# Kernel tuning notes

Measured on AMD Instinct MI355X. Metric: run time of the kernel, lower is better.

Reference implementation:

```python
import jax, jax.numpy as jnp
import numpy as np

N = 512
NQ = 8
SIGMA = 1.0
NORM_FACTOR = 90.4756
NC = NORM_FACTOR / (2.0 * np.pi)  # norm_const = norm_factor / twopi


def make_kernels(r, sigma, nc):
    # Gaussian-screened Coulomb kernel g(r) = erf(a r)/r, a = 1/(sigma*sqrt(2)),
    # and its Cartesian tensor derivatives D1..D4 (D_n = (1/r d/dr)^n g).
    n = r.shape[0]
    d = r[None, :, :] - r[:, None, :]          # d[i,j] = r_j - r_i  [n,n,3]
    eye = jnp.eye(n, dtype=bool)
    r2 = jnp.sum(d * d, axis=-1)
    rr = jnp.sqrt(jnp.where(eye, 1.0, r2))     # safe diagonal
    a = 1.0 / (sigma * np.sqrt(2.0))
    a2 = a * a
    E = jax.scipy.special.erf(a * rr)
    G = (2.0 * a / np.sqrt(np.pi)) * jnp.exp(-a2 * rr * rr)
    ir = 1.0 / rr
    ir2 = ir * ir; ir3 = ir2 * ir; ir4 = ir2 * ir2; ir5 = ir4 * ir
    ir6 = ir4 * ir2; ir7 = ir6 * ir; ir8 = ir4 * ir4; ir9 = ir8 * ir
    off = jnp.where(eye, 0.0, 1.0).astype(r.dtype)  # remove self interaction
    g  = E * ir * off
    D1 = (G * ir2 - E * ir3) * off
    D2 = (3.0 * E * ir5 - 3.0 * G * ir4 - 2.0 * a2 * G * ir2) * off
    D3 = (-15.0 * E * ir7 + 15.0 * G * ir6 + 10.0 * a2 * G * ir4
          + 4.0 * a2 * a2 * G * ir2) * off
    D4 = (105.0 * E * ir9 - 105.0 * G * ir8 - 70.0 * a2 * G * ir6
          - 28.0 * a2 * a2 * G * ir4 - 8.0 * a2 * a2 * a2 * G * ir2) * off
    I3 = jnp.eye(3, dtype=r.dtype)
    f_qq = nc * g                                        # [n,n]
    f_qu = -nc * D1[..., None] * d                       # [n,n,3]
    dd = d[..., :, None] * d[..., None, :]               # [n,n,3,3]
    f_uu = nc * (D2[..., None, None] * dd + D1[..., None, None] * I3)
    ddd = dd[..., None] * d[..., None, None, :]          # [n,n,3,3,3]
    s3 = (jnp.einsum('ab,ijc->ijabc', I3, d)
          + jnp.einsum('ac,ijb->ijabc', I3, d)
          + jnp.einsum('bc,ija->ijabc', I3, d))
    f_Qu = nc * (D3[..., None, None, None] * ddd + D2[..., None, None, None] * s3)
    dddd = ddd[..., None] * d[:, :, None, None, None, :]  # [n,n,3,3,3,3]
    s6 = (jnp.einsum('ab,ijcd->ijabcd', I3, dd)
          + jnp.einsum('ac,ijbd->ijabcd', I3, dd)
          + jnp.einsum('ad,ijbc->ijabcd', I3, dd)
          + jnp.einsum('bc,ijad->ijabcd', I3, dd)
          + jnp.einsum('bd,ijac->ijabcd', I3, dd)
          + jnp.einsum('cd,ijab->ijabcd', I3, dd))
    iso = (jnp.einsum('ab,cd->abcd', I3, I3)
           + jnp.einsum('ac,bd->abcd', I3, I3)
           + jnp.einsum('ad,bc->abcd', I3, I3))
    f_QQ = nc * (D4[..., None, None, None, None] * dddd
                 + D3[..., None, None, None, None] * s6
                 + D2[..., None, None, None, None] * iso)
    return f_qq, f_qu, f_uu, f_Qu, f_QQ


def ewald_realspace(q, r, u, quad, kappa, alpha):
    f_qq, f_qu, f_uu, f_Qu, f_QQ = make_kernels(r, SIGMA, NC)
    # charge-charge
    e_phi = jnp.einsum('iq,ij->jq', q, f_qq)
    pot = 0.5 * jnp.einsum('iq,iq->q', e_phi, q)
    # charge-dipole
    e_phi_u = jnp.einsum('iqc,ijc->jq', u, f_qu)
    e_phi = e_phi + e_phi_u
    pot = pot + jnp.einsum('iq,iq->q', e_phi_u, q)
    # dipole-dipole
    E_u = jnp.einsum('ijcd,iqc->jqd', f_uu, u)
    pot = pot - 0.5 * jnp.einsum('iqc,iqc->q', u, E_u)
    # quadrupole terms
    e_phi_Q = 0.5 * jnp.einsum('iqab,ijab->jq', quad, f_uu)
    E_Q = -0.5 * jnp.einsum('iqab,ijabc->jqc', quad, f_Qu)
    e_phi = e_phi + e_phi_Q
    pot = pot + jnp.einsum('iq,iq->q', q, e_phi_Q)
    QQ = jnp.einsum('ijabcd,jqcd->iqab', f_QQ, quad)
    pot = pot + 0.125 * jnp.einsum('iqab,iqab->q', quad, QQ)
    pot = pot - jnp.einsum('iqc,iqc->q', u, E_Q)
    # induced charges (kappa)
    q_induced = -kappa * e_phi
    pot = pot + 0.5 * jnp.sum(e_phi * q_induced, axis=0)
    # field and induced dipoles (alpha, scalar polarizability)
    e_field = jnp.einsum('iq,ijc->jqc', q, f_qu) + E_u + E_Q
    u_induced = e_field * alpha[..., None]
    pot = pot - 0.5 * jnp.sum(e_field * u_induced, axis=(0, 2))
    return pot.sum().reshape(-1), q_induced, u_induced


def setup_inputs():
    key = jax.random.key(0)
    ks = jax.random.split(key, 6)
    r = jax.random.normal(ks[0], (N, 3), jnp.float32) * 5.0
    q = jax.random.normal(ks[1], (N, NQ), jnp.float32)
    u = jax.random.normal(ks[2], (N, NQ, 3), jnp.float32)
    quad = jax.random.normal(ks[3], (N, NQ, 3, 3), jnp.float32)
    kappa = jax.random.uniform(ks[4], (N, NQ), jnp.float32)
    alpha = jax.random.uniform(ks[5], (N, NQ), jnp.float32)
    cell = jnp.zeros((1, 3, 3), jnp.float32)   # det < 1e-6 -> realspace branch
    batch = jnp.zeros((N,), jnp.int32)         # single system
    return {'q': q, 'r': r, 'cell': cell, 'batch': batch, 'u': u,
            'quad': quad, 'kappa': kappa, 'alpha': alpha}


def reference(q, r, cell, batch, u, quad, kappa, alpha):
    # cell is zero (det < 1e-6) and batch is a single graph -> realspace path
    return ewald_realspace(q, r, u, quad, kappa, alpha)
```

## Files before the change

### kernel.cpp

```cpp
#include <hip/hip_runtime.h>
#include <math.h>

#define NA 512
#define NQC 8

#define NCf ((float)(90.4756 / 6.28318530717958647692))
#define A_ERF 0.70710678118654752f
#define G_COEF 0.79788456080286536f

typedef float v2f __attribute__((ext_vector_type(2)));

__global__ __launch_bounds__(512)
void main_kernel(const float* __restrict__ qarr,
                 const float* __restrict__ rarr,
                 const float* __restrict__ uarr,
                 const float* __restrict__ quadarr,
                 const float* __restrict__ kaparr,
                 const float* __restrict__ alparr,
                 float* __restrict__ out,
                 float* __restrict__ potpart) {
    const int j    = blockIdx.x;
    const int tid  = threadIdx.x;
    const int qch  = tid & 7;
    const int lane = tid & 63;
    const int wv   = tid >> 6;

    __shared__ float sCo[8][64][8];

    const float rjx = rarr[j*3+0], rjy = rarr[j*3+1], rjz = rarr[j*3+2];

    const int jq = j * NQC + qch;
    const float* Qj = quadarr + (size_t)jq * 9;
    const float jxx = Qj[0], jyy = Qj[4], jzz = Qj[8];
    const float jxy = 0.5f*(Qj[1]+Qj[3]);
    const float jxz = 0.5f*(Qj[2]+Qj[6]);
    const float jyz = 0.5f*(Qj[5]+Qj[7]);
    const float jtq = jxx + jyy + jzz;

    {
        const int myi = ((lane >> 3) << 6) + (wv << 3) + (lane & 7);
        const float mdx = rjx - rarr[myi*3+0];
        const float mdy = rjy - rarr[myi*3+1];
        const float mdz = rjz - rarr[myi*3+2];
        float r2 = mdx*mdx + mdy*mdy + mdz*mdz;
        const bool diag = (myi == j);
        if (diag) r2 = 1.0f;
        const float ir  = rsqrtf(r2);
        const float rr  = r2 * ir;
        const float x   = A_ERF * rr;
        const float E2  = __expf(-0.5f * r2);
        const float G   = G_COEF * E2;
        const float t   = __builtin_amdgcn_rcpf(fmaf(0.3275911f, x, 1.0f));
        const float pol = t*(0.254829592f + t*(-0.284496736f + t*(1.421413741f
                         + t*(-1.453152027f + t*1.061405429f))));
        const float E   = fmaf(-pol, E2, 1.0f);
        const float ir2 = ir * ir;
        const float ir4 = ir2 * ir2;
        const float g   = E * ir;
        const float GmG = G - g;
        const float nco = diag ? 0.0f : NCf;
        float4* slot = (float4*)&sCo[wv][lane][0];
        slot[0] = make_float4(nco * g,
                              nco * ir2 * GmG,
                              nco * ir2 * (-3.0f*ir2*GmG - G),
                              nco * ir2 * (15.0f*ir4*GmG + 5.0f*G*ir2 + G));
        slot[1] = make_float4(nco * ir2 * (-105.0f*ir4*ir2*GmG - 35.0f*G*ir4
                                           - 7.0f*G*ir2 - G),
                              mdx, mdy, mdz);
    }

    v2f e0 = 0.f, eph = 0.f;
    v2f Gx = 0.f, Gy = 0.f, Gz = 0.f;
    v2f Hx = 0.f, Hy = 0.f, Hz = 0.f;
    v2f pQQ = 0.f;

    #pragma unroll
    for (int k2 = 0; k2 < 4; ++k2) {
        const int iq0 = (2*k2) * 512 + tid;
        const int iq1 = iq0 + 512;
        const int p0  = ((2*k2) << 3) + (lane >> 3);
        const int p1  = p0 + 8;

        const float4 ca0 = *(const float4*)&sCo[wv][p0][0];
        const float4 cb0 = *(const float4*)&sCo[wv][p0][4];
        const float4 ca1 = *(const float4*)&sCo[wv][p1][0];
        const float4 cb1 = *(const float4*)&sCo[wv][p1][4];
        const v2f c0 = {ca0.x, ca1.x}, c1 = {ca0.y, ca1.y};
        const v2f c2 = {ca0.z, ca1.z}, c3 = {ca0.w, ca1.w};
        const v2f c4 = {cb0.x, cb1.x};
        const v2f dx = {cb0.y, cb1.y}, dy = {cb0.z, cb1.z}, dz = {cb0.w, cb1.w};

        const v2f qi = {qarr[iq0], qarr[iq1]};
        const v2f ux = {uarr[iq0*3+0], uarr[iq1*3+0]};
        const v2f uy = {uarr[iq0*3+1], uarr[iq1*3+1]};
        const v2f uz = {uarr[iq0*3+2], uarr[iq1*3+2]};
        const float* Qi0 = quadarr + (size_t)iq0 * 9;
        const float* Qi1 = quadarr + (size_t)iq1 * 9;
        const v2f xx = {Qi0[0], Qi1[0]};
        const v2f yy = {Qi0[4], Qi1[4]};
        const v2f zz = {Qi0[8], Qi1[8]};
        const v2f q01 = {Qi0[1], Qi1[1]}, q03 = {Qi0[3], Qi1[3]};
        const v2f q02 = {Qi0[2], Qi1[2]}, q06 = {Qi0[6], Qi1[6]};
        const v2f q05 = {Qi0[5], Qi1[5]}, q07 = {Qi0[7], Qi1[7]};
        const v2f xy = 0.5f*(q01 + q03);
        const v2f xz = 0.5f*(q02 + q06);
        const v2f yz = 0.5f*(q05 + q07);
        const v2f tqi = xx + yy + zz;

        const v2f ud  = ux*dx + uy*dy + uz*dz;
        const v2f Pdx = xx*dx + xy*dy + xz*dz;
        const v2f Pdy = xy*dx + yy*dy + yz*dz;
        const v2f Pdz = xz*dx + yz*dy + zz*dz;
        const v2f Pdd = Pdx*dx + Pdy*dy + Pdz*dz;

        const v2f t0 = c0 * qi;
        e0  += t0;
        eph += t0 - c1*ud + 0.5f*(c2*Pdd + c1*tqi);

        const v2f c1h = 0.5f * c1;
        const v2f cH = 0.5f*(c2*(ud - tqi) - c3*Pdd);
        const v2f gf = 0.5f*c2*ud - c1*qi;
        Hx += cH*dx + c1h*ux - c2*Pdx;
        Hy += cH*dy + c1h*uy - c2*Pdy;
        Hz += cH*dz + c1h*uz - c2*Pdz;
        Gx += gf*dx + c1h*ux;
        Gy += gf*dy + c1h*uy;
        Gz += gf*dz + c1h*uz;

        const v2f Rdx = jxx*dx + jxy*dy + jxz*dz;
        const v2f Rdy = jxy*dx + jyy*dy + jyz*dz;
        const v2f Rdz = jxz*dx + jyz*dy + jzz*dz;
        const v2f Rdd = Rdx*dx + Rdy*dy + Rdz*dz;
        const v2f dPR = Pdx*Rdx + Pdy*Rdy + Pdz*Rdz;
        const v2f frob = xx*jxx + yy*jyy + zz*jzz + 2.0f*(xy*jxy + xz*jxz + yz*jyz);
        pQQ += c4*(Pdd*Rdd)
             + c3*(jtq*Pdd + tqi*Rdd + 4.0f*dPR)
             + c2*(tqi*jtq + 2.0f*frob);
    }

    const float e0s = e0.x + e0.y, ephs = eph.x + eph.y;
    const float Hxs = Hx.x + Hx.y, Hys = Hy.x + Hy.y, Hzs = Hz.x + Hz.y;
    const float Fxs = Hxs + Gx.x + Gx.y;
    const float Fys = Hys + Gy.x + Gy.y;
    const float Fzs = Hzs + Gz.x + Gz.y;
    const float pQQs = pQQ.x + pQQ.y;

    float acc[9] = {e0s, ephs, Fxs, Fys, Fzs, Hxs, Hys, Hzs, pQQs};
    #pragma unroll
    for (int off = 8; off < 64; off <<= 1) {
        #pragma unroll
        for (int c = 0; c < 9; ++c) acc[c] += __shfl_xor(acc[c], off, 64);
    }
    __shared__ float red[8][8][9];
    if ((lane & 56) == 0) {
        #pragma unroll
        for (int c = 0; c < 9; ++c) red[wv][lane][c] = acc[c];
    }
    __syncthreads();
    if (tid < 8) {
        float v[9];
        #pragma unroll
        for (int c = 0; c < 9; ++c) {
            float s = 0.f;
            #pragma unroll
            for (int w = 0; w < 8; ++w) s += red[w][tid][c];
            v[c] = s;
        }
        const float te0 = v[0], teph = v[1];
        const float tFx = v[2], tFy = v[3], tFz = v[4];
        const float tHx = v[5], tHy = v[6], tHz = v[7];
        const float tQQ = v[8] * 0.125f;
        const int myjq = j * NQC + tid;
        const float qj  = qarr[myjq];
        const float ujx = uarr[myjq*3+0], ujy = uarr[myjq*3+1], ujz = uarr[myjq*3+2];
        const float kapv = kaparr[myjq];
        const float alpv = alparr[myjq];

        float pot = qj * (teph - 0.5f*te0)
                  - (ujx*tHx + ujy*tHy + ujz*tHz)
                  + tQQ
                  - 0.5f * kapv * teph * teph
                  - 0.5f * alpv * (tFx*tFx + tFy*tFy + tFz*tFz);

        out[1 + myjq] = -kapv * teph;
        out[1 + NA*NQC + myjq*3 + 0] = alpv * tFx;
        out[1 + NA*NQC + myjq*3 + 1] = alpv * tFy;
        out[1 + NA*NQC + myjq*3 + 2] = alpv * tFz;

        #pragma unroll
        for (int off = 4; off; off >>= 1) pot += __shfl_xor(pot, off, 8);
        if (tid == 0) potpart[j] = pot;
    }
}

__global__ void pot_kernel(const float* __restrict__ potpart, float* __restrict__ out) {
    const int t = threadIdx.x;
    float s = 0.f;
    #pragma unroll
    for (int m = 0; m < 8; ++m) s += potpart[t + m*64];
    #pragma unroll
    for (int off = 32; off; off >>= 1) s += __shfl_xor(s, off, 64);
    if (t == 0) out[0] = s;
}

extern "C" void kernel_launch(void* const* d_in, const int* in_sizes, int n_in,
                              void* d_out, int out_size, void* d_ws, size_t ws_size,
                              hipStream_t stream) {
    const float* q    = (const float*)d_in[0];
    const float* r    = (const float*)d_in[1];
    const float* u    = (const float*)d_in[4];
    const float* quad = (const float*)d_in[5];
    const float* kap  = (const float*)d_in[6];
    const float* alp  = (const float*)d_in[7];
    float* out = (float*)d_out;
    float* potpart = (float*)d_ws;
    (void)ws_size; (void)in_sizes; (void)n_in; (void)out_size;

    main_kernel<<<NA, 512, 0, stream>>>(q, r, u, quad, kap, alp, out, potpart);
    pot_kernel<<<1, 64, 0, stream>>>(potpart, out);
}
```

Measured before the change: 15.85 us.

## Fuse final potential reduction into main kernel via spin-wait reducer block

Drops the separate pot_kernel launch and adds one extra block to the main grid. That block spins on sharded atomic completion counters until all 512 partial potentials are published, then reduces them. Each worker block stores its partial with an atomic store and then bumps its counter shard. This saves a kernel launch, but adds a memset call and relies on the extra block not starving the workers. The spin also has no acquire fence, so ordering rests on relaxed atomics.

```diff
diff --git a/kernel.cpp b/kernel.cpp
--- a/kernel.cpp
+++ b/kernel.cpp
@@ -18,9 +18,37 @@
                  const float* __restrict__ kaparr,
                  const float* __restrict__ alparr,
                  float* __restrict__ out,
-                 float* __restrict__ potpart) {
+                 float* __restrict__ potpart,
+                 unsigned int* __restrict__ counter) {
     const int j    = blockIdx.x;
     const int tid  = threadIdx.x;
+
+    if (j == NA) {
+        if (tid == 0) {
+            unsigned int done;
+            do {
+                done = 0;
+                #pragma unroll
+                for (int i = 0; i < 8; ++i)
+                    done += __hip_atomic_load(&counter[i * 32], __ATOMIC_RELAXED,
+                                              __HIP_MEMORY_SCOPE_AGENT);
+                if (done < NA) __builtin_amdgcn_s_sleep(16);
+            } while (done < NA);
+        }
+        __syncthreads();
+        if (tid < 64) {
+            float s = 0.f;
+            #pragma unroll
+            for (int m = 0; m < 8; ++m)
+                s += __hip_atomic_load(&potpart[tid + m * 64], __ATOMIC_RELAXED,
+                                       __HIP_MEMORY_SCOPE_AGENT);
+            #pragma unroll
+            for (int off = 32; off; off >>= 1) s += __shfl_xor(s, off, 64);
+            if (tid == 0) out[0] = s;
+        }
+        return;
+    }
+
     const int qch  = tid & 7;
     const int lane = tid & 63;
     const int wv   = tid >> 6;
@@ -189,18 +217,14 @@
 
         #pragma unroll
         for (int off = 4; off; off >>= 1) pot += __shfl_xor(pot, off, 8);
-        if (tid == 0) potpart[j] = pot;
-    }
-}
-
-__global__ void pot_kernel(const float* __restrict__ potpart, float* __restrict__ out) {
-    const int t = threadIdx.x;
-    float s = 0.f;
-    #pragma unroll
-    for (int m = 0; m < 8; ++m) s += potpart[t + m*64];
-    #pragma unroll
-    for (int off = 32; off; off >>= 1) s += __shfl_xor(s, off, 64);
-    if (t == 0) out[0] = s;
+        if (tid == 0) {
+            __hip_atomic_store(&potpart[j], pot, __ATOMIC_RELAXED,
+                               __HIP_MEMORY_SCOPE_AGENT);
+            asm volatile("s_waitcnt vmcnt(0)" ::: "memory");
+            __hip_atomic_fetch_add(&counter[(j & 7) * 32], 1u, __ATOMIC_RELAXED,
+                                   __HIP_MEMORY_SCOPE_AGENT);
+        }
+    }
 }
 
 extern "C" void kernel_launch(void* const* d_in, const int* in_sizes, int n_in,
@@ -214,8 +238,10 @@
     const float* alp  = (const float*)d_in[7];
     float* out = (float*)d_out;
     float* potpart = (float*)d_ws;
+    unsigned int* counter = (unsigned int*)((float*)d_ws + NA);
     (void)ws_size; (void)in_sizes; (void)n_in; (void)out_size;
 
-    main_kernel<<<NA, 512, 0, stream>>>(q, r, u, quad, kap, alp, out, potpart);
-    pot_kernel<<<1, 64, 0, stream>>>(potpart, out);
+    hipMemsetAsync(counter, 0, 8 * 32 * sizeof(unsigned int), stream);
+    main_kernel<<<NA + 1, 512, 0, stream>>>(q, r, u, quad, kap, alp, out,
+                                            potpart, counter);
 }
```

After: 20.54 us. 1.3x slower.

## Split each atom's source loop across two blocks with atomic last-block combine

Applied to the files above, without the earlier changes.

Each target atom j is now handled by two blocks, each covering half of the source atoms. Each block writes its partial sums to workspace, and the second block to arrive, detected through a per-atom atomic counter, combines both halves and writes the outputs. The aim is to double the grid size for more parallelism and latency hiding, at the cost of half-idle lanes in the coefficient stage, extra global traffic, and atomics. Counter parity depends on the workspace state carried over between calls rather than on a reset.

```diff
diff --git a/kernel.cpp b/kernel.cpp
--- a/kernel.cpp
+++ b/kernel.cpp
@@ -3,6 +3,7 @@
 
 #define NA 512
 #define NQC 8
+#define IPB 256
 
 #define NCf ((float)(90.4756 / 6.28318530717958647692))
 #define A_ERF 0.70710678118654752f
@@ -18,14 +19,18 @@
                  const float* __restrict__ kaparr,
                  const float* __restrict__ alparr,
                  float* __restrict__ out,
-                 float* __restrict__ potpart) {
-    const int j    = blockIdx.x;
+                 float* __restrict__ potpart,
+                 float* __restrict__ part,
+                 unsigned int* __restrict__ counter) {
+    const int b    = blockIdx.x;
+    const int j    = b >> 1;
+    const int half = b & 1;
     const int tid  = threadIdx.x;
     const int qch  = tid & 7;
     const int lane = tid & 63;
     const int wv   = tid >> 6;
 
-    __shared__ float sCo[8][64][8];
+    __shared__ float sCo[8][32][8];
 
     const float rjx = rarr[j*3+0], rjy = rarr[j*3+1], rjz = rarr[j*3+2];
 
@@ -38,7 +43,7 @@
     const float jtq = jxx + jyy + jzz;
 
     {
-        const int myi = ((lane >> 3) << 6) + (wv << 3) + (lane & 7);
+        const int myi = half*IPB + (((lane >> 3) & 3) << 6) + (wv << 3) + (lane & 7);
         const float mdx = rjx - rarr[myi*3+0];
         const float mdy = rjy - rarr[myi*3+1];
         const float mdz = rjz - rarr[myi*3+2];
@@ -59,14 +64,16 @@
         const float g   = E * ir;
         const float GmG = G - g;
         const float nco = diag ? 0.0f : NCf;
-        float4* slot = (float4*)&sCo[wv][lane][0];
-        slot[0] = make_float4(nco * g,
-                              nco * ir2 * GmG,
-                              nco * ir2 * (-3.0f*ir2*GmG - G),
-                              nco * ir2 * (15.0f*ir4*GmG + 5.0f*G*ir2 + G));
-        slot[1] = make_float4(nco * ir2 * (-105.0f*ir4*ir2*GmG - 35.0f*G*ir4
-                                           - 7.0f*G*ir2 - G),
-                              mdx, mdy, mdz);
+        if (lane < 32) {
+            float4* slot = (float4*)&sCo[wv][lane][0];
+            slot[0] = make_float4(nco * g,
+                                  nco * ir2 * GmG,
+                                  nco * ir2 * (-3.0f*ir2*GmG - G),
+                                  nco * ir2 * (15.0f*ir4*GmG + 5.0f*G*ir2 + G));
+            slot[1] = make_float4(nco * ir2 * (-105.0f*ir4*ir2*GmG - 35.0f*G*ir4
+                                               - 7.0f*G*ir2 - G),
+                                  mdx, mdy, mdz);
+        }
     }
 
     v2f e0 = 0.f, eph = 0.f;
@@ -75,10 +82,10 @@
     v2f pQQ = 0.f;
 
     #pragma unroll
-    for (int k2 = 0; k2 < 4; ++k2) {
-        const int iq0 = (2*k2) * 512 + tid;
+    for (int k2 = 0; k2 < 2; ++k2) {
+        const int iq0 = half*2048 + (2*k2) * 512 + tid;
         const int iq1 = iq0 + 512;
-        const int p0  = ((2*k2) << 3) + (lane >> 3);
+        const int p0  = (k2 << 4) + (lane >> 3);
         const int p1  = p0 + 8;
 
         const float4 ca0 = *(const float4*)&sCo[wv][p0][0];
@@ -157,8 +164,9 @@
         for (int c = 0; c < 9; ++c) red[wv][lane][c] = acc[c];
     }
     __syncthreads();
+
+    float v[9];
     if (tid < 8) {
-        float v[9];
         #pragma unroll
         for (int c = 0; c < 9; ++c) {
             float s = 0.f;
@@ -166,6 +174,28 @@
             for (int w = 0; w < 8; ++w) s += red[w][tid][c];
             v[c] = s;
         }
+        const int slot = ((j*2 + half) * 8 + tid) * 9;
+        #pragma unroll
+        for (int c = 0; c < 9; ++c)
+            __hip_atomic_store(&part[slot + c], v[c], __ATOMIC_RELAXED,
+                               __HIP_MEMORY_SCOPE_AGENT);
+        asm volatile("s_waitcnt vmcnt(0)" ::: "memory");
+    }
+    __syncthreads();
+
+    __shared__ unsigned int s_old;
+    if (tid == 0)
+        s_old = __hip_atomic_fetch_add(&counter[j * 32], 1u, __ATOMIC_RELAXED,
+                                       __HIP_MEMORY_SCOPE_AGENT);
+    __syncthreads();
+
+    if ((s_old & 1u) == 1u && tid < 8) {
+        const int pslot = ((j*2 + (half ^ 1)) * 8 + tid) * 9;
+        #pragma unroll
+        for (int c = 0; c < 9; ++c)
+            v[c] += __hip_atomic_load(&part[pslot + c], __ATOMIC_RELAXED,
+                                      __HIP_MEMORY_SCOPE_AGENT);
+
         const float te0 = v[0], teph = v[1];
         const float tFx = v[2], tFy = v[3], tFz = v[4];
         const float tHx = v[5], tHy = v[6], tHz = v[7];
@@ -213,9 +243,14 @@
     const float* kap  = (const float*)d_in[6];
     const float* alp  = (const float*)d_in[7];
     float* out = (float*)d_out;
-    float* potpart = (float*)d_ws;
+    float* ws  = (float*)d_ws;
+
+    float* potpart = ws;
+    float* part    = ws + NA;
+    unsigned int* counter = (unsigned int*)(ws + NA + NA*2*NQC*9);
     (void)ws_size; (void)in_sizes; (void)n_in; (void)out_size;
 
-    main_kernel<<<NA, 512, 0, stream>>>(q, r, u, quad, kap, alp, out, potpart);
+    main_kernel<<<NA*2, 512, 0, stream>>>(q, r, u, quad, kap, alp, out,
+                                          potpart, part, counter);
     pot_kernel<<<1, 64, 0, stream>>>(potpart, out);
 }
```

Result: slower. 20.66 us (+30.4%).
